# Optimization experiments

Hardware: AMD Instinct MI355X
Metric: run time of the kernel (lower is better)

Reference implementation:

```python
import jax, jax.numpy as jnp
import numpy as np

B, N, HID = 1, 2048, 1024
H, WK, WV = 16, 64, 64
DH = HID // H  # 64


def setup_inputs() -> dict:
    key = jax.random.key(0)
    ks = jax.random.split(key, 10)
    s = 0.02
    return {
        "hidden_states": jax.random.normal(ks[0], (B, N, HID), jnp.float32),
        "attention_mask": jnp.ones((B, N), jnp.float32),
        "Wq": jax.random.normal(ks[1], (HID, HID), jnp.float32) * s,
        "bq": jnp.zeros((HID,), jnp.float32),
        "Wk": jax.random.normal(ks[2], (HID, HID), jnp.float32) * s,
        "bk": jnp.zeros((HID,), jnp.float32),
        "Wv": jax.random.normal(ks[3], (HID, HID), jnp.float32) * s,
        "bv": jnp.zeros((HID,), jnp.float32),
        # Conv1D(2*WK+1, DH, bias=False): weight [nx=DH, nf=2*WK+1]
        "W_rel_k": jax.random.normal(ks[4], (DH, 2 * WK + 1), jnp.float32) * s,
        # relative_pos_val: [2*WV+1, DH]
        "W_rel_v": jax.random.normal(ks[5], (2 * WV + 1, DH), jnp.float32) * s,
    }


def _attention(hidden_states, attention_mask, Wq, bq, Wk, bk, Wv, bv, W_rel_k, W_rel_v):
    b, n, _ = hidden_states.shape

    def heads(x):  # [B,N,HID] -> [B,H,N,DH]
        return x.reshape(b, n, H, DH).transpose(0, 2, 1, 3)

    q = heads(hidden_states @ Wq + bq)
    k = heads(hidden_states @ Wk + bk)
    v = heads(hidden_states @ Wv + bv)

    scores = jnp.einsum("bhid,bhjd->bhij", q, k)  # [B,H,N,N]

    # --- relative-position key bias: bias[i, j] = q_i . w_{j-i+WK} for |j-i|<=WK ---
    a_k = jnp.einsum("bhid,dw->bhiw", q, W_rel_k)  # [B,H,N,2*WK+1]
    rows = jnp.arange(n)
    slot = rows[None, :] - rows[:, None] + WK       # [N,N] relative slot j-i+WK
    valid_k = (slot >= 0) & (slot <= 2 * WK)
    bias = a_k[:, :, rows[:, None], jnp.clip(slot, 0, 2 * WK)]  # [B,H,N,N]
    scores = scores + jnp.where(valid_k, bias, 0.0)

    scores = scores / np.float32(np.sqrt(DH))  # temperature == 1.0

    # extended attention mask: (1 - mask) * dtype_min added to scores
    ext = (1.0 - attention_mask)[:, None, None, :] * jnp.finfo(scores.dtype).min
    scores = scores + ext

    probs = jax.nn.softmax(scores, axis=-1)  # [B,H,N,N]

    ctx = jnp.einsum("bhij,bhjd->bhid", probs, v)  # [B,H,N,DH]

    # --- relative-position value: band[i, r] = probs[i, i-WV+r]; ctx += band @ W_rel_v ---
    offs = jnp.arange(2 * WV + 1)
    kpos = rows[:, None] - WV + offs[None, :]       # [N, 2*WV+1] absolute key position
    valid_v = (kpos >= 0) & (kpos < n)
    band = probs[:, :, rows[:, None], jnp.clip(kpos, 0, n - 1)]  # [B,H,N,2*WV+1]
    band = jnp.where(valid_v, band, 0.0)
    ctx = ctx + jnp.einsum("bhiw,wd->bhid", band, W_rel_v)

    # merge heads -> [B,N,HID]
    return ctx.transpose(0, 2, 1, 3).reshape(b, n, HID)


def reference(hidden_states, attention_mask, Wq, bq, Wk, bk, Wv, bv, W_rel_k, W_rel_v):
    return _attention(hidden_states, attention_mask, Wq, bq, Wk, bk, Wv, bv, W_rel_k, W_rel_v)
```

## Files before the change

### kernel.cpp

```cpp
#include <hip/hip_runtime.h>
#include <hip/hip_bf16.h>

#define NSEQ 2048
#define HIDDIM 1024
#define NH 16
#define DHEAD 64
#define NW 129
#define AKS 132

typedef float          f32x4 __attribute__((ext_vector_type(4)));
typedef _Float16       f16x4 __attribute__((ext_vector_type(4)));
typedef _Float16       f16x8 __attribute__((ext_vector_type(8)));
typedef unsigned short u16x8 __attribute__((ext_vector_type(8)));
typedef unsigned short u16;

__device__ __forceinline__ float b2f(u16 u){ return __uint_as_float(((unsigned)u) << 16); }
__device__ __forceinline__ float ld_any(const void* p, long idx, int flag){
  return flag ? b2f(((const u16*)p)[idx]) : ((const float*)p)[idx];
}
__device__ __forceinline__ int dtype_flag(const void* mask){
  return (((const unsigned*)mask)[0] == 0x3F800000u) ? 0 : 1;
}

#define GLOAD_LDS16(gp, lp) \
  __builtin_amdgcn_global_load_lds((const __attribute__((address_space(1))) unsigned int*)(gp), \
                                   (__attribute__((address_space(3))) unsigned int*)(lp), 16, 0, 0)

static const size_t OFF_Q    = 0;
static const size_t OFF_K    = (size_t)4  << 20;
static const size_t OFF_VT   = (size_t)8  << 20;
static const size_t OFF_WT   = (size_t)12 << 20;
static const size_t OFF_AK   = (size_t)18 << 20;
static const size_t OFF_M    = OFF_AK + (size_t)NH * NSEQ * AKS * 4;
static const size_t OFF_L    = OFF_M + (size_t)2 * NH * NSEQ * 4;
static const size_t OFF_CTXP = OFF_L + (size_t)2 * NH * NSEQ * 4;
static const size_t OFF_HSF  = OFF_CTXP + (size_t)2 * NSEQ * HIDDIM * 4;
static const size_t OFF_BIAS = OFF_HSF + (size_t)NSEQ * HIDDIM * 2;
static const size_t OFF_EXT  = OFF_BIAS + 3 * 1024 * 4;
static const size_t OFF_WRKT = OFF_EXT + (size_t)NSEQ * 4;
static const size_t OFF_WRVT = OFF_WRKT + (size_t)144 * 72 * 2;

__global__ void prep_kernel(const void* __restrict__ hs, const void* __restrict__ mask,
                            const void* __restrict__ bq, const void* __restrict__ bk,
                            const void* __restrict__ bv, const void* __restrict__ wrk,
                            const void* __restrict__ wrv,
                            const void* __restrict__ Wq, const void* __restrict__ Wk,
                            const void* __restrict__ Wv,
                            _Float16* __restrict__ hsf, float* __restrict__ biasf,
                            float* __restrict__ extf, _Float16* __restrict__ wrkT16,
                            _Float16* __restrict__ wrvT16, _Float16* __restrict__ Wt){
  __shared__ __attribute__((aligned(16))) _Float16 tile[64][65];
  const int flag = dtype_flag(mask);
  const int b = blockIdx.x;
  const int t = threadIdx.x;
  if (b < 1024){
    const long base = (long)(b * 256 + t) * 8;
    f16x8 o;
    if (flag){
      u16x8 v = *(const u16x8*)((const u16*)hs + base);
#pragma unroll
      for (int e = 0; e < 8; e++) o[e] = (_Float16)b2f(v[e]);
    } else {
      f32x4 a = *(const f32x4*)((const float*)hs + base);
      f32x4 c = *(const f32x4*)((const float*)hs + base + 4);
#pragma unroll
      for (int e = 0; e < 4; e++){ o[e] = (_Float16)a[e]; o[4 + e] = (_Float16)c[e]; }
    }
    *(f16x8*)(hsf + base) = o;
    return;
  }
  if (b < 1121){
    const int idx = (b - 1024) * 256 + t;
    if (idx < 1024)            biasf[idx] = ld_any(bq, idx, flag);
    else if (idx < 2048)       biasf[idx] = ld_any(bk, idx - 1024, flag);
    else if (idx < 3072)       biasf[idx] = ld_any(bv, idx - 2048, flag);
    else if (idx < 5120)       extf[idx - 3072] = (1.f - ld_any(mask, idx - 3072, flag)) * -1.0e30f;
    else if (idx < 5120 + 144 * 72){
      int i2 = idx - 5120;
      int w = i2 / 72, d = i2 - w * 72;
      wrkT16[i2] = (w < NW && d < 64) ? (_Float16)ld_any(wrk, (long)d * NW + w, flag) : (_Float16)0.f;
    } else if (idx < 5120 + 144 * 72 + 64 * 144){
      int i3 = idx - (5120 + 144 * 72);
      int d = i3 / 144, w = i3 - d * 144;
      wrvT16[i3] = (w < NW) ? (_Float16)ld_any(wrv, (long)w * 64 + d, flag) : (_Float16)0.f;
    }
    return;
  }
  const int b2 = b - 1121;
  const int z = b2 >> 8, rem = b2 & 255;
  const void* src = (z == 0) ? Wq : ((z == 1) ? Wk : Wv);
  _Float16* dst = Wt + (size_t)z * 1024 * 1024;
  const int o0 = (rem & 15) * 64, k0 = (rem >> 4) * 64;
#pragma unroll
  for (int c = 0; c < 2; c++){
    int idx = t + 256 * c;
    int r = idx >> 3, c8 = (idx & 7) * 8;
    long off = (long)(k0 + r) * 1024 + o0 + c8;
    if (flag){
      u16x8 v = *(const u16x8*)((const u16*)src + off);
#pragma unroll
      for (int e = 0; e < 8; e++) tile[r][c8 + e] = (_Float16)b2f(v[e]);
    } else {
      f32x4 a = *(const f32x4*)((const float*)src + off);
      f32x4 bb = *(const f32x4*)((const float*)src + off + 4);
#pragma unroll
      for (int e = 0; e < 4; e++){ tile[r][c8 + e] = (_Float16)a[e]; tile[r][c8 + 4 + e] = (_Float16)bb[e]; }
    }
  }
  __syncthreads();
#pragma unroll
  for (int c = 0; c < 2; c++){
    int idx = t + 256 * c;
    int orow = idx >> 3, k8 = (idx & 7) * 8;
    f16x8 v;
#pragma unroll
    for (int e = 0; e < 8; e++) v[e] = tile[k8 + e][orow];
    *(f16x8*)(dst + (size_t)(o0 + orow) * 1024 + k0 + k8) = v;
  }
}

__launch_bounds__(512, 4)
__global__ void qkv_kernel(const _Float16* __restrict__ hsf, const _Float16* __restrict__ Wt,
                           const float* __restrict__ biasf,
                           _Float16* __restrict__ Qf, _Float16* __restrict__ Kf,
                           _Float16* __restrict__ Vtf){
  __shared__ __attribute__((aligned(16))) _Float16 As[2 * 64 * 64];
  __shared__ __attribute__((aligned(16))) _Float16 Bs[2 * 128 * 64];
  const int z = blockIdx.z;
  const _Float16* Wz = Wt + (size_t)z * 1024 * 1024;
  const int o0 = blockIdx.x * 128, m0 = blockIdx.y * 64;
  const int t = threadIdx.x, lane = t & 63, wave = t >> 6;
  const int wm = wave >> 2, wn = wave & 3;
  const int q = lane >> 4, ln = lane & 15;

  auto stage = [&](int nb, int k0){
    {
      const int row = t >> 3, slot = t & 7;
      const int c8 = slot ^ (row & 7);
      GLOAD_LDS16(hsf + (size_t)(m0 + row) * 1024 + k0 + (c8 << 3),
                  (_Float16*)As + nb * 4096 + (wave << 9));
    }
#pragma unroll
    for (int p = 0; p < 2; p++){
      const int g = p * 512 + t;
      const int row = g >> 3, slot = g & 7;
      const int c8 = slot ^ (row & 7);
      GLOAD_LDS16(Wz + (size_t)(o0 + row) * 1024 + k0 + (c8 << 3),
                  (_Float16*)Bs + nb * 8192 + ((p * 8 + wave) << 9));
    }
  };

  f32x4 acc[2][2];
#pragma unroll
  for (int a = 0; a < 2; a++)
#pragma unroll
    for (int b = 0; b < 2; b++) acc[a][b] = (f32x4){0.f, 0.f, 0.f, 0.f};

  stage(0, 0);
  __syncthreads();
  int cur = 0;
  for (int k0 = 0; k0 < 1024; k0 += 64){
    if (k0 + 64 < 1024) stage(cur ^ 1, k0 + 64);
    const _Float16* Ac = (const _Float16*)As + cur * 4096;
    const _Float16* Bc = (const _Float16*)Bs + cur * 8192;
    __builtin_amdgcn_s_setprio(1);
#pragma unroll
    for (int ks = 0; ks < 2; ks++){
      f16x8 af[2], bf[2];
#pragma unroll
      for (int mt = 0; mt < 2; mt++){
        int row = wm * 32 + mt * 16 + ln;
        af[mt] = *(const f16x8*)&Ac[(row << 6) + (((ks * 4 + q) ^ (row & 7)) << 3)];
      }
#pragma unroll
      for (int nt = 0; nt < 2; nt++){
        int row = wn * 32 + nt * 16 + ln;
        bf[nt] = *(const f16x8*)&Bc[(row << 6) + (((ks * 4 + q) ^ (row & 7)) << 3)];
      }
#pragma unroll
      for (int mt = 0; mt < 2; mt++)
#pragma unroll
        for (int nt = 0; nt < 2; nt++)
          acc[mt][nt] = __builtin_amdgcn_mfma_f32_16x16x32_f16(af[mt], bf[nt], acc[mt][nt], 0, 0, 0);
    }
    __builtin_amdgcn_s_setprio(0);
    __syncthreads();
    cur ^= 1;
  }
  const float sc = (z == 0) ? 0.125f : 1.0f;
#pragma unroll
  for (int nt = 0; nt < 2; nt++){
    int o = o0 + wn * 32 + nt * 16 + ln;
    float bval = biasf[z * 1024 + o];
    int hh = o >> 6, dd = o & 63;
#pragma unroll
    for (int mt = 0; mt < 2; mt++){
      int nb = m0 + wm * 32 + mt * 16 + q * 4;
      if (z == 2){
        f16x4 pk;
#pragma unroll
        for (int r = 0; r < 4; r++) pk[r] = (_Float16)(acc[mt][nt][r] + bval);
        *(f16x4*)(Vtf + (size_t)(hh * 64 + dd) * 2048 + nb) = pk;
      } else {
        _Float16* dstp = (z == 0) ? Qf : Kf;
#pragma unroll
        for (int r = 0; r < 4; r++)
          dstp[(size_t)(hh * 2048 + nb + r) * 64 + dd] = (_Float16)((acc[mt][nt][r] + bval) * sc);
      }
    }
  }
}

__launch_bounds__(256, 2)
__global__ void ak_kernel(const _Float16* __restrict__ Qf, const _Float16* __restrict__ wrkT16,
                          float* __restrict__ ak){
  __shared__ __attribute__((aligned(16))) _Float16 WrkT[144 * 72];
  const int h = blockIdx.y;
  const int i0 = blockIdx.x * 64;
  const int t = threadIdx.x, lane = t & 63, wave = t >> 6;
  const int q = lane >> 4, ln = lane & 15;
  {
    const f16x8* srcv = (const f16x8*)wrkT16;
    f16x8* dstv = (f16x8*)WrkT;
#pragma unroll
    for (int c = 0; c < 6; c++){
      int v = c * 256 + t;
      if (v < 144 * 72 / 8) dstv[v] = srcv[v];
    }
  }
  __syncthreads();
  const int row = i0 + wave * 16 + ln;
  f16x8 afr[2];
#pragma unroll
  for (int ks = 0; ks < 2; ks++)
    afr[ks] = *(const f16x8*)(Qf + (size_t)(h * 2048 + row) * 64 + ks * 32 + q * 8);
  f32x4 acc[9];
#pragma unroll
  for (int b = 0; b < 9; b++) acc[b] = (f32x4){0.f, 0.f, 0.f, 0.f};
#pragma unroll
  for (int nt = 0; nt < 9; nt++){
    f16x8 bfr0 = *(const f16x8*)&WrkT[(nt * 16 + ln) * 72 + q * 8];
    f16x8 bfr1 = *(const f16x8*)&WrkT[(nt * 16 + ln) * 72 + 32 + q * 8];
    acc[nt] = __builtin_amdgcn_mfma_f32_16x16x32_f16(afr[0], bfr0, acc[nt], 0, 0, 0);
    acc[nt] = __builtin_amdgcn_mfma_f32_16x16x32_f16(afr[1], bfr1, acc[nt], 0, 0, 0);
  }
#pragma unroll
  for (int nt = 0; nt < 9; nt++){
    int w = nt * 16 + ln;
    if (w > 128) continue;
    int ib = i0 + wave * 16 + q * 4;
#pragma unroll
    for (int r = 0; r < 4; r++)
      ak[(size_t)(h * 2048 + ib + r) * AKS + w] = acc[nt][r];
  }
}

__launch_bounds__(256, 4)
__global__ void flash_kernel(const float* __restrict__ extf,
                             const _Float16* __restrict__ Qf, const _Float16* __restrict__ Kf,
                             const _Float16* __restrict__ Vtf, float* akm,
                             float* __restrict__ ctxpart, float* __restrict__ mws,
                             float* __restrict__ lws){
  __shared__ __attribute__((aligned(16))) _Float16 Ks[2 * 64 * 64];
  __shared__ __attribute__((aligned(16))) _Float16 Vts[2 * 64 * 64];
  __shared__ __attribute__((aligned(16))) float Exts[1024];
  __shared__ int eflags[4];
  const int h = blockIdx.x, qt = blockIdx.y, jh = blockIdx.z;
  const int t = threadIdx.x, lane = t & 63, wave = t >> 6;
  const int q = lane >> 4, ln = lane & 15;
  const int ibase = qt * 64 + wave * 16;
  const int i = ibase + ln;
  const int jb = jh * 1024;
  const int phase = (h + 3 * qt + 8 * jh) & 15;

  auto stageK = [&](int nb, int jn){
#pragma unroll
    for (int p = 0; p < 2; p++){
      const int g = p * 256 + t;
      const int row = g >> 3, slot = g & 7;
      const int col8 = slot ^ (row & 7);
      GLOAD_LDS16(Kf + (((size_t)(h * 2048 + jn + row)) << 6) + (col8 << 3),
                  (_Float16*)Ks + nb * 4096 + ((p * 4 + wave) << 9));
    }
  };
  auto stageV = [&](int nb, int jn){
#pragma unroll
    for (int p = 0; p < 2; p++){
      const int g = p * 256 + t;
      const int row = g >> 3, slot = g & 7;
      const int col8 = slot ^ (row & 7);
      GLOAD_LDS16(Vtf + (((size_t)(h * 64 + row)) << 11) + jn + (col8 << 3),
                  (_Float16*)Vts + nb * 4096 + ((p * 4 + wave) << 9));
    }
  };

  const int ds7 = ln & 7;
  const _Float16* kb0 = (const _Float16*)Ks + (ln << 6) + ((q ^ ds7) << 3);
  const _Float16* kb1 = (const _Float16*)Ks + (ln << 6) + (((q + 4) ^ ds7) << 3);
  const _Float16* vb0 = (const _Float16*)Vts + (ln << 6) + (((0 | (q >> 1)) ^ ds7) << 3) + ((q & 1) << 2);
  const _Float16* vb1 = (const _Float16*)Vts + (ln << 6) + (((2 | (q >> 1)) ^ ds7) << 3) + ((q & 1) << 2);
  const _Float16* vb2 = (const _Float16*)Vts + (ln << 6) + (((4 | (q >> 1)) ^ ds7) << 3) + ((q & 1) << 2);
  const _Float16* vb3 = (const _Float16*)Vts + (ln << 6) + (((6 | (q >> 1)) ^ ds7) << 3) + ((q & 1) << 2);

  f16x8 qfrag[2];
  {
    const _Float16* qrow = Qf + (size_t)(h * 2048 + i) * 64;
    qfrag[0] = *(const f16x8*)(qrow + q * 8);
    qfrag[1] = *(const f16x8*)(qrow + 32 + q * 8);
  }
  f32x4 accc[4];
#pragma unroll
  for (int dt = 0; dt < 4; dt++) accc[dt] = (f32x4){0.f, 0.f, 0.f, 0.f};
  float m_i = -1.0e30f, l_i = 0.f;
  float* akrow = akm + (size_t)(h * 2048 + i) * AKS;
  f32x4 s[4];

  auto qk = [&](int PK){
    __builtin_amdgcn_s_setprio(1);
#pragma unroll
    for (int mt = 0; mt < 4; mt++){
      f16x8 kf0 = *(const f16x8*)(kb0 + PK * 4096 + mt * 1024);
      f16x8 kf1 = *(const f16x8*)(kb1 + PK * 4096 + mt * 1024);
      f32x4 zz = (f32x4){0.f, 0.f, 0.f, 0.f};
      zz = __builtin_amdgcn_mfma_f32_16x16x32_f16(kf0, qfrag[0], zz, 0, 0, 0);
      zz = __builtin_amdgcn_mfma_f32_16x16x32_f16(kf1, qfrag[1], zz, 0, 0, 0);
      s[mt] = zz;
    }
    __builtin_amdgcn_s_setprio(0);
  };

  auto jof = [&](int x){ return jb + ((x + phase) & 15) * 64; };

  bool nz = false;
#pragma unroll
  for (int c = 0; c < 4; c++){
    float e = extf[jb + c * 256 + t];
    Exts[c * 256 + t] = e;
    nz |= (e != 0.f);
  }
  {
    unsigned long long bz = __ballot(nz);
    if (lane == 0) eflags[wave] = (bz != 0ull) ? 1 : 0;
  }
  stageK(0, jof(0));
  __syncthreads();
  const bool extNZ = (eflags[0] | eflags[1] | eflags[2] | eflags[3]) != 0;
  stageV(0, jof(0));
  stageK(1, jof(1));
  qk(0);
  __syncthreads();

  auto body = [&](int t_, int PV_, int PK1, bool last){
    const int j0 = jof(t_);
    if (!last){
      stageV(PK1, jof(t_ + 1));
      if (t_ < 14) stageK(PV_, jof(t_ + 2));
    }
    const bool band = (j0 <= ibase + 79) && (j0 + 63 >= ibase - 64);
    const int je = (t_ + phase) & 15;
    if (band){
#pragma unroll
      for (int mt = 0; mt < 4; mt++){
        f32x4 ev = *(const f32x4*)&Exts[je * 64 + mt * 16 + (q << 2)];
#pragma unroll
        for (int r = 0; r < 4; r++){
          float x = s[mt][r];
          int w = j0 + mt * 16 + (q << 2) + r - i + 64;
          if ((unsigned)w <= 128u){
            x = x + akrow[w] + ev[r];
            akrow[w] = x;
          } else {
            x = x + ev[r];
          }
          s[mt][r] = x;
        }
      }
    } else if (extNZ){
#pragma unroll
      for (int mt = 0; mt < 4; mt++){
        f32x4 ev = *(const f32x4*)&Exts[je * 64 + mt * 16 + (q << 2)];
#pragma unroll
        for (int r = 0; r < 4; r++) s[mt][r] += ev[r];
      }
    }
    float a0 = fmaxf(fmaxf(s[0][0], s[0][1]), fmaxf(s[0][2], s[0][3]));
    float a1 = fmaxf(fmaxf(s[1][0], s[1][1]), fmaxf(s[1][2], s[1][3]));
    float a2 = fmaxf(fmaxf(s[2][0], s[2][1]), fmaxf(s[2][2], s[2][3]));
    float a3 = fmaxf(fmaxf(s[3][0], s[3][1]), fmaxf(s[3][2], s[3][3]));
    float tmax = fmaxf(fmaxf(a0, a1), fmaxf(a2, a3));
    tmax = fmaxf(tmax, __shfl_xor(tmax, 16, 64));
    tmax = fmaxf(tmax, __shfl_xor(tmax, 32, 64));
    float mnew = fmaxf(m_i, tmax);
    if (!__all(tmax <= m_i)){
      float alpha = __expf(m_i - mnew);
      l_i *= alpha;
#pragma unroll
      for (int dt = 0; dt < 4; dt++)
#pragma unroll
        for (int r = 0; r < 4; r++) accc[dt][r] *= alpha;
    }
    m_i = mnew;
    float ps[4][4];
#pragma unroll
    for (int mt = 0; mt < 4; mt++)
#pragma unroll
      for (int r = 0; r < 4; r++) ps[mt][r] = __expf(s[mt][r] - mnew);
    f16x4 pf[4];
#pragma unroll
    for (int mt = 0; mt < 4; mt++)
#pragma unroll
      for (int r = 0; r < 4; r++) pf[mt][r] = (_Float16)ps[mt][r];
    float t0 = (ps[0][0] + ps[0][1]) + (ps[0][2] + ps[0][3]);
    float t1 = (ps[1][0] + ps[1][1]) + (ps[1][2] + ps[1][3]);
    float t2 = (ps[2][0] + ps[2][1]) + (ps[2][2] + ps[2][3]);
    float t3 = (ps[3][0] + ps[3][1]) + (ps[3][2] + ps[3][3]);
    float tsum = (t0 + t1) + (t2 + t3);
    tsum += __shfl_xor(tsum, 16, 64);
    tsum += __shfl_xor(tsum, 32, 64);
    l_i += tsum;
    if (!last) qk(PK1);
    __builtin_amdgcn_s_setprio(1);
#pragma unroll
    for (int dt = 0; dt < 4; dt++){
      f16x4 vf0 = *(const f16x4*)(vb0 + PV_ * 4096 + dt * 1024);
      f16x4 vf1 = *(const f16x4*)(vb1 + PV_ * 4096 + dt * 1024);
      f16x4 vf2 = *(const f16x4*)(vb2 + PV_ * 4096 + dt * 1024);
      f16x4 vf3 = *(const f16x4*)(vb3 + PV_ * 4096 + dt * 1024);
      accc[dt] = __builtin_amdgcn_mfma_f32_16x16x16f16(vf0, pf[0], accc[dt], 0, 0, 0);
      accc[dt] = __builtin_amdgcn_mfma_f32_16x16x16f16(vf1, pf[1], accc[dt], 0, 0, 0);
      accc[dt] = __builtin_amdgcn_mfma_f32_16x16x16f16(vf2, pf[2], accc[dt], 0, 0, 0);
      accc[dt] = __builtin_amdgcn_mfma_f32_16x16x16f16(vf3, pf[3], accc[dt], 0, 0, 0);
    }
    __builtin_amdgcn_s_setprio(0);
    __syncthreads();
  };

  for (int tt = 0; tt < 8; tt++){
    body(2 * tt,     0, 1, false);
    body(2 * tt + 1, 1, 0, tt == 7);
  }

  float* cdst = ctxpart + (size_t)jh * NSEQ * HIDDIM;
#pragma unroll
  for (int dt = 0; dt < 4; dt++)
    *(f32x4*)(cdst + (size_t)i * 1024 + h * 64 + dt * 16 + q * 4) = accc[dt];
  if (q == 0){
    mws[jh * NH * NSEQ + h * 2048 + i] = m_i;
    lws[jh * NH * NSEQ + h * 2048 + i] = l_i;
  }
}

__launch_bounds__(256, 2)
__global__ void finish_kernel(const float* __restrict__ sband, const float* __restrict__ mws,
                              const float* __restrict__ lws, const _Float16* __restrict__ wrvT16,
                              const float* __restrict__ ctxpart, float* __restrict__ out){
  __shared__ __attribute__((aligned(16))) _Float16 WrvT[64 * 144];
  __shared__ __attribute__((aligned(16))) _Float16 pT[144 * 72];
  __shared__ __attribute__((aligned(16))) float sM[64], sIL[64], sC0[64], sC1[64];
  const int qt = blockIdx.x, h = blockIdx.y;
  const int i0 = qt * 64;
  const int t = threadIdx.x, lane = t & 63, wave = t >> 6;
  const int q = lane >> 4, ln = lane & 15;
  {
    const f16x8* srcv = (const f16x8*)wrvT16;
    f16x8* dstv = (f16x8*)WrvT;
#pragma unroll
    for (int c = 0; c < 5; c++){
      int v = c * 256 + t;
      if (v < 64 * 144 / 8) dstv[v] = srcv[v];
    }
  }
  if (t < 64){
    int i = i0 + t;
    float m0 = mws[h * 2048 + i],            m1 = mws[NH * NSEQ + h * 2048 + i];
    float l0 = lws[h * 2048 + i],            l1 = lws[NH * NSEQ + h * 2048 + i];
    float M = fmaxf(m0, m1);
    float a0 = __expf(m0 - M), a1 = __expf(m1 - M);
    float L = a0 * l0 + a1 * l1;
    float iL = 1.f / L;
    sM[t] = M; sIL[t] = iL; sC0[t] = a0 * iL; sC1[t] = a1 * iL;
  }
  __syncthreads();
  for (int ii = 0; ii < 16; ii++){
    int il = wave * 16 + ii;
    float Mv = sM[il], ILv = sIL[il];
    const float* srow = sband + (size_t)(h * 2048 + i0 + il) * AKS;
#pragma unroll
    for (int c = 0; c < 3; c++){
      int w = lane + 64 * c;
      if (w < 144){
        float p = (w < NW) ? __expf(srow[w] - Mv) * ILv : 0.f;
        pT[w * 72 + il] = (_Float16)p;
      }
    }
  }
  __syncthreads();
  f32x4 acc[4];
#pragma unroll
  for (int mt = 0; mt < 4; mt++) acc[mt] = (f32x4){0.f, 0.f, 0.f, 0.f};
#pragma unroll
  for (int ks = 0; ks < 9; ks++){
    f16x4 bfr;
#pragma unroll
    for (int j = 0; j < 4; j++) bfr[j] = pT[(ks * 16 + q * 4 + j) * 72 + wave * 16 + ln];
#pragma unroll
    for (int mt = 0; mt < 4; mt++){
      f16x4 afr = *(const f16x4*)&WrvT[(mt * 16 + ln) * 144 + ks * 16 + q * 4];
      acc[mt] = __builtin_amdgcn_mfma_f32_16x16x16f16(afr, bfr, acc[mt], 0, 0, 0);
    }
  }
  const int i = i0 + wave * 16 + ln;
  const float c0 = sC0[wave * 16 + ln], c1 = sC1[wave * 16 + ln];
  const float* p0 = ctxpart;
  const float* p1 = ctxpart + (size_t)NSEQ * HIDDIM;
#pragma unroll
  for (int mt = 0; mt < 4; mt++){
    size_t off = (size_t)i * 1024 + h * 64 + mt * 16 + q * 4;
    f32x4 A0 = *(const f32x4*)(p0 + off);
    f32x4 A1 = *(const f32x4*)(p1 + off);
    f32x4 o4;
#pragma unroll
    for (int r = 0; r < 4; r++) o4[r] = c0 * A0[r] + c1 * A1[r] + acc[mt][r];
    *(f32x4*)(out + off) = o4;
  }
}

extern "C" void kernel_launch(void* const* d_in, const int* in_sizes, int n_in,
                              void* d_out, int out_size, void* d_ws, size_t ws_size,
                              hipStream_t stream){
  const void* hs   = d_in[0];
  const void* mask = d_in[1];
  const void* Wq   = d_in[2];
  const void* bq   = d_in[3];
  const void* Wk   = d_in[4];
  const void* bk   = d_in[5];
  const void* Wv   = d_in[6];
  const void* bv   = d_in[7];
  const void* Wrk  = d_in[8];
  const void* Wrv  = d_in[9];
  float* out = (float*)d_out;

  char* ws = (char*)d_ws;
  _Float16* Qf    = (_Float16*)(ws + OFF_Q);
  _Float16* Kf    = (_Float16*)(ws + OFF_K);
  _Float16* Vtf   = (_Float16*)(ws + OFF_VT);
  _Float16* Wt    = (_Float16*)(ws + OFF_WT);
  float*    akp   = (float*)   (ws + OFF_AK);
  float*    mp    = (float*)   (ws + OFF_M);
  float*    lp    = (float*)   (ws + OFF_L);
  float*    ctxp  = (float*)   (ws + OFF_CTXP);
  _Float16* hsf   = (_Float16*)(ws + OFF_HSF);
  float*    biasf = (float*)   (ws + OFF_BIAS);
  float*    extf  = (float*)   (ws + OFF_EXT);
  _Float16* wrkT16= (_Float16*)(ws + OFF_WRKT);
  _Float16* wrvT16= (_Float16*)(ws + OFF_WRVT);

  prep_kernel     <<<dim3(1889),       256, 0, stream>>>(hs, mask, bq, bk, bv, Wrk, Wrv,
                                                         Wq, Wk, Wv,
                                                         hsf, biasf, extf, wrkT16, wrvT16, Wt);
  qkv_kernel      <<<dim3(8, 32, 3),   512, 0, stream>>>(hsf, Wt, biasf, Qf, Kf, Vtf);
  ak_kernel       <<<dim3(32, 16),     256, 0, stream>>>(Qf, wrkT16, akp);
  flash_kernel    <<<dim3(16, 32, 2),  256, 0, stream>>>(extf, Qf, Kf, Vtf, akp, ctxp, mp, lp);
  finish_kernel   <<<dim3(32, 16),     256, 0, stream>>>(akp, mp, lp, wrvT16, ctxp, out);
}
```

Baseline: 182.4 us.

## Fuse relative-key projection into QKV epilogue and store split-K context in fp16

Removes the separate ak_kernel. The Q-projection blocks stage their scaled Q tile in shared memory and compute the relative-key band projection there using MFMA. This saves one launch and a global re-read of Q, but adds tail work only to the z==0 blocks, which unbalances the grid. Separately, the flash kernel's partial context accumulators are written and read back as fp16 instead of fp32, halving that intermediate traffic at some precision cost before the final combine.

```diff
diff --git a/kernel.cpp b/kernel.cpp
--- a/kernel.cpp
+++ b/kernel.cpp
@@ -121,9 +121,9 @@
 
 __launch_bounds__(512, 4)
 __global__ void qkv_kernel(const _Float16* __restrict__ hsf, const _Float16* __restrict__ Wt,
-                           const float* __restrict__ biasf,
+                           const float* __restrict__ biasf, const _Float16* __restrict__ wrkT16,
                            _Float16* __restrict__ Qf, _Float16* __restrict__ Kf,
-                           _Float16* __restrict__ Vtf){
+                           _Float16* __restrict__ Vtf, float* __restrict__ akp){
   __shared__ __attribute__((aligned(16))) _Float16 As[2 * 64 * 64];
   __shared__ __attribute__((aligned(16))) _Float16 Bs[2 * 128 * 64];
   const int z = blockIdx.z;
@@ -188,14 +188,18 @@
     cur ^= 1;
   }
   const float sc = (z == 0) ? 0.125f : 1.0f;
+  _Float16* Qs = (_Float16*)As;
+  _Float16* Wl = (_Float16*)Bs;
 #pragma unroll
   for (int nt = 0; nt < 2; nt++){
-    int o = o0 + wn * 32 + nt * 16 + ln;
+    int ol = wn * 32 + nt * 16 + ln;
+    int o = o0 + ol;
     float bval = biasf[z * 1024 + o];
     int hh = o >> 6, dd = o & 63;
 #pragma unroll
     for (int mt = 0; mt < 2; mt++){
-      int nb = m0 + wm * 32 + mt * 16 + q * 4;
+      int ml = wm * 32 + mt * 16 + q * 4;
+      int nb = m0 + ml;
       if (z == 2){
         f16x4 pk;
 #pragma unroll
@@ -204,54 +208,50 @@
       } else {
         _Float16* dstp = (z == 0) ? Qf : Kf;
 #pragma unroll
-        for (int r = 0; r < 4; r++)
-          dstp[(size_t)(hh * 2048 + nb + r) * 64 + dd] = (_Float16)((acc[mt][nt][r] + bval) * sc);
-      }
-    }
-  }
-}
-
-__launch_bounds__(256, 2)
-__global__ void ak_kernel(const _Float16* __restrict__ Qf, const _Float16* __restrict__ wrkT16,
-                          float* __restrict__ ak){
-  __shared__ __attribute__((aligned(16))) _Float16 WrkT[144 * 72];
-  const int h = blockIdx.y;
-  const int i0 = blockIdx.x * 64;
-  const int t = threadIdx.x, lane = t & 63, wave = t >> 6;
-  const int q = lane >> 4, ln = lane & 15;
-  {
-    const f16x8* srcv = (const f16x8*)wrkT16;
-    f16x8* dstv = (f16x8*)WrkT;
-#pragma unroll
-    for (int c = 0; c < 6; c++){
-      int v = c * 256 + t;
-      if (v < 144 * 72 / 8) dstv[v] = srcv[v];
-    }
-  }
-  __syncthreads();
-  const int row = i0 + wave * 16 + ln;
-  f16x8 afr[2];
-#pragma unroll
-  for (int ks = 0; ks < 2; ks++)
-    afr[ks] = *(const f16x8*)(Qf + (size_t)(h * 2048 + row) * 64 + ks * 32 + q * 8);
-  f32x4 acc[9];
-#pragma unroll
-  for (int b = 0; b < 9; b++) acc[b] = (f32x4){0.f, 0.f, 0.f, 0.f};
-#pragma unroll
-  for (int nt = 0; nt < 9; nt++){
-    f16x8 bfr0 = *(const f16x8*)&WrkT[(nt * 16 + ln) * 72 + q * 8];
-    f16x8 bfr1 = *(const f16x8*)&WrkT[(nt * 16 + ln) * 72 + 32 + q * 8];
-    acc[nt] = __builtin_amdgcn_mfma_f32_16x16x32_f16(afr[0], bfr0, acc[nt], 0, 0, 0);
-    acc[nt] = __builtin_amdgcn_mfma_f32_16x16x32_f16(afr[1], bfr1, acc[nt], 0, 0, 0);
-  }
-#pragma unroll
-  for (int nt = 0; nt < 9; nt++){
-    int w = nt * 16 + ln;
-    if (w > 128) continue;
-    int ib = i0 + wave * 16 + q * 4;
-#pragma unroll
-    for (int r = 0; r < 4; r++)
-      ak[(size_t)(h * 2048 + ib + r) * AKS + w] = acc[nt][r];
+        for (int r = 0; r < 4; r++){
+          _Float16 v16 = (_Float16)((acc[mt][nt][r] + bval) * sc);
+          dstp[(size_t)(hh * 2048 + nb + r) * 64 + dd] = v16;
+          if (z == 0) Qs[(ol >> 6) * 4096 + (ml + r) * 64 + dd] = v16;
+        }
+      }
+    }
+  }
+  if (z == 0){
+    {
+      const f16x8* srcv = (const f16x8*)wrkT16;
+      f16x8* dstv = (f16x8*)Wl;
+#pragma unroll
+      for (int c = 0; c < 3; c++){
+        int v = c * 512 + t;
+        if (v < 144 * 72 / 8) dstv[v] = srcv[v];
+      }
+    }
+    __syncthreads();
+    const int hl = wave >> 2, mb = wave & 3;
+    f16x8 afr[2];
+#pragma unroll
+    for (int ks = 0; ks < 2; ks++)
+      afr[ks] = *(const f16x8*)&Qs[hl * 4096 + (mb * 16 + ln) * 64 + ks * 32 + q * 8];
+    f32x4 aacc[9];
+#pragma unroll
+    for (int b = 0; b < 9; b++) aacc[b] = (f32x4){0.f, 0.f, 0.f, 0.f};
+#pragma unroll
+    for (int nt = 0; nt < 9; nt++){
+      f16x8 bfr0 = *(const f16x8*)&Wl[(nt * 16 + ln) * 72 + q * 8];
+      f16x8 bfr1 = *(const f16x8*)&Wl[(nt * 16 + ln) * 72 + 32 + q * 8];
+      aacc[nt] = __builtin_amdgcn_mfma_f32_16x16x32_f16(afr[0], bfr0, aacc[nt], 0, 0, 0);
+      aacc[nt] = __builtin_amdgcn_mfma_f32_16x16x32_f16(afr[1], bfr1, aacc[nt], 0, 0, 0);
+    }
+    const int hg = blockIdx.x * 2 + hl;
+#pragma unroll
+    for (int nt = 0; nt < 9; nt++){
+      int w = nt * 16 + ln;
+      if (w > 128) continue;
+      int ib = m0 + mb * 16 + q * 4;
+#pragma unroll
+      for (int r = 0; r < 4; r++)
+        akp[(size_t)(hg * 2048 + ib + r) * AKS + w] = aacc[nt][r];
+    }
   }
 }
 
@@ -259,7 +259,7 @@
 __global__ void flash_kernel(const float* __restrict__ extf,
                              const _Float16* __restrict__ Qf, const _Float16* __restrict__ Kf,
                              const _Float16* __restrict__ Vtf, float* akm,
-                             float* __restrict__ ctxpart, float* __restrict__ mws,
+                             _Float16* __restrict__ ctxpart, float* __restrict__ mws,
                              float* __restrict__ lws){
   __shared__ __attribute__((aligned(16))) _Float16 Ks[2 * 64 * 64];
   __shared__ __attribute__((aligned(16))) _Float16 Vts[2 * 64 * 64];
@@ -440,10 +440,14 @@
     body(2 * tt + 1, 1, 0, tt == 7);
   }
 
-  float* cdst = ctxpart + (size_t)jh * NSEQ * HIDDIM;
-#pragma unroll
-  for (int dt = 0; dt < 4; dt++)
-    *(f32x4*)(cdst + (size_t)i * 1024 + h * 64 + dt * 16 + q * 4) = accc[dt];
+  _Float16* cdst = ctxpart + (size_t)jh * NSEQ * HIDDIM;
+#pragma unroll
+  for (int dt = 0; dt < 4; dt++){
+    f16x4 pk;
+#pragma unroll
+    for (int r = 0; r < 4; r++) pk[r] = (_Float16)accc[dt][r];
+    *(f16x4*)(cdst + (size_t)i * 1024 + h * 64 + dt * 16 + q * 4) = pk;
+  }
   if (q == 0){
     mws[jh * NH * NSEQ + h * 2048 + i] = m_i;
     lws[jh * NH * NSEQ + h * 2048 + i] = l_i;
@@ -453,7 +457,7 @@
 __launch_bounds__(256, 2)
 __global__ void finish_kernel(const float* __restrict__ sband, const float* __restrict__ mws,
                               const float* __restrict__ lws, const _Float16* __restrict__ wrvT16,
-                              const float* __restrict__ ctxpart, float* __restrict__ out){
+                              const _Float16* __restrict__ ctxpart, float* __restrict__ out){
   __shared__ __attribute__((aligned(16))) _Float16 WrvT[64 * 144];
   __shared__ __attribute__((aligned(16))) _Float16 pT[144 * 72];
   __shared__ __attribute__((aligned(16))) float sM[64], sIL[64], sC0[64], sC1[64];
@@ -511,16 +515,16 @@
   }
   const int i = i0 + wave * 16 + ln;
   const float c0 = sC0[wave * 16 + ln], c1 = sC1[wave * 16 + ln];
-  const float* p0 = ctxpart;
-  const float* p1 = ctxpart + (size_t)NSEQ * HIDDIM;
+  const _Float16* p0 = ctxpart;
+  const _Float16* p1 = ctxpart + (size_t)NSEQ * HIDDIM;
 #pragma unroll
   for (int mt = 0; mt < 4; mt++){
     size_t off = (size_t)i * 1024 + h * 64 + mt * 16 + q * 4;
-    f32x4 A0 = *(const f32x4*)(p0 + off);
-    f32x4 A1 = *(const f32x4*)(p1 + off);
+    f16x4 A0 = *(const f16x4*)(p0 + off);
+    f16x4 A1 = *(const f16x4*)(p1 + off);
     f32x4 o4;
 #pragma unroll
-    for (int r = 0; r < 4; r++) o4[r] = c0 * A0[r] + c1 * A1[r] + acc[mt][r];
+    for (int r = 0; r < 4; r++) o4[r] = c0 * (float)A0[r] + c1 * (float)A1[r] + acc[mt][r];
     *(f32x4*)(out + off) = o4;
   }
 }
@@ -548,7 +552,7 @@
   float*    akp   = (float*)   (ws + OFF_AK);
   float*    mp    = (float*)   (ws + OFF_M);
   float*    lp    = (float*)   (ws + OFF_L);
-  float*    ctxp  = (float*)   (ws + OFF_CTXP);
+  _Float16* ctxp  = (_Float16*)(ws + OFF_CTXP);
   _Float16* hsf   = (_Float16*)(ws + OFF_HSF);
   float*    biasf = (float*)   (ws + OFF_BIAS);
   float*    extf  = (float*)   (ws + OFF_EXT);
@@ -558,8 +562,8 @@
   prep_kernel     <<<dim3(1889),       256, 0, stream>>>(hs, mask, bq, bk, bv, Wrk, Wrv,
                                                          Wq, Wk, Wv,
                                                          hsf, biasf, extf, wrkT16, wrvT16, Wt);
-  qkv_kernel      <<<dim3(8, 32, 3),   512, 0, stream>>>(hsf, Wt, biasf, Qf, Kf, Vtf);
-  ak_kernel       <<<dim3(32, 16),     256, 0, stream>>>(Qf, wrkT16, akp);
+  qkv_kernel      <<<dim3(8, 32, 3),   512, 0, stream>>>(hsf, Wt, biasf, wrkT16,
+                                                         Qf, Kf, Vtf, akp);
   flash_kernel    <<<dim3(16, 32, 2),  256, 0, stream>>>(extf, Qf, Kf, Vtf, akp, ctxp, mp, lp);
   finish_kernel   <<<dim3(32, 16),     256, 0, stream>>>(akp, mp, lp, wrvT16, ctxp, out);
 }
```

After: 173.9 us, median of 2. 1.05x faster.
